# Kernel optimization log

Hardware: AMD Instinct MI355X
Metric: run time of the kernel (lower is better)

## Reference

```python
import jax, jax.numpy as jnp
import numpy as np
from jax.ops import segment_sum

N_NODES = 50000
N_EDGES = 150000
IN_FEATS = 512
OUT_FEATS = 512


def setup_inputs() -> dict:
    key = jax.random.key(0)
    k1, k2, k3, k4 = jax.random.split(key, 4)
    x = jax.random.normal(k1, (N_NODES, IN_FEATS), dtype=jnp.float32)
    src = jax.random.randint(k2, (N_EDGES,), 0, N_NODES, dtype=jnp.int64)
    dst = jax.random.randint(k3, (N_EDGES,), 0, N_NODES, dtype=jnp.int64)
    # Xavier-uniform init like reset_parameters
    limit = float(np.sqrt(6.0 / (IN_FEATS + OUT_FEATS)))
    W = jax.random.uniform(k4, (IN_FEATS, OUT_FEATS), dtype=jnp.float32,
                           minval=-limit, maxval=limit)
    b = jnp.zeros((OUT_FEATS,), dtype=jnp.float32)
    return {"x": x, "src": src, "dst": dst, "W": W, "b": b}


def reference(x, src, dst, W, b):
    # DGL GraphConv with norm='both':
    #   out = relu( D_dst^{-1/2} A D_src^{-1/2} X W + b )
    # Dropout is identity in eval mode (training=False).
    ones = jnp.ones((src.shape[0],), dtype=x.dtype)
    deg_out = segment_sum(ones, src, num_segments=N_NODES)  # source out-degree
    deg_in = segment_sum(ones, dst, num_segments=N_NODES)   # dest in-degree
    norm_src = jnp.where(deg_out > 0, deg_out, 1.0) ** -0.5  # [N]
    norm_dst = jnp.where(deg_in > 0, deg_in, 1.0) ** -0.5    # [N]

    h = x * norm_src[:, None]                         # [N, in]
    agg = segment_sum(h[src], dst, num_segments=N_NODES)  # scatter-add over edges
    agg = agg * norm_dst[:, None]                     # [N, in]
    out = agg @ W + b                                 # [N, out]
    return jax.nn.relu(out)
```

## Files before the change

kernel.cpp:

```cpp
#include <hip/hip_runtime.h>
#include <hip/hip_bf16.h>

#define N_NODES 50000
#define N_PAD   50048
#define N_EDGES 150000
#define F 512
#define BM 128
#define BN 128
#define BK 64
#define NBLK 196

typedef __attribute__((ext_vector_type(4))) float f32x4;
typedef __attribute__((ext_vector_type(4))) unsigned int u32x4;
typedef __attribute__((ext_vector_type(2))) unsigned int u32x2;

__device__ __forceinline__ unsigned short f2bf(float f) {
    unsigned int u = __float_as_uint(f);
    return (unsigned short)((u + 0x7fffu + ((u >> 16) & 1u)) >> 16);
}
__device__ __forceinline__ unsigned int pack2(float a, float b) {
    return (unsigned int)f2bf(a) | ((unsigned int)f2bf(b) << 16);
}
__device__ __forceinline__ void gload16(const void* g, void* l) {
    __builtin_amdgcn_global_load_lds(
        (const __attribute__((address_space(1))) unsigned int*)g,
        (__attribute__((address_space(3))) unsigned int*)l, 16, 0, 0);
}

__global__ void __launch_bounds__(256) crd_deg(const int* __restrict__ src,
                                               const int* __restrict__ dst,
                                               int* __restrict__ hist) {
    int e = blockIdx.x * 256 + threadIdx.x;
    if (e < N_EDGES) {
        atomicAdd(&hist[src[e]], 1);
        atomicAdd(&hist[N_NODES + dst[e]], 1);
    }
}

__global__ void __launch_bounds__(256) crd_norm(const int* __restrict__ hist,
                                                float* __restrict__ norms) {
    int i = blockIdx.x * 256 + threadIdx.x;
    if (i < 2 * N_NODES) {
        int d = hist[i];
        norms[i] = rsqrtf((float)(d > 0 ? d : 1));
    }
}

__global__ void __launch_bounds__(256) crd_bsum(const int* __restrict__ hist_in,
                                                int* __restrict__ bsum) {
    __shared__ int s[256];
    int t = threadIdx.x;
    int i = blockIdx.x * 256 + t;
    s[t] = (i < N_NODES) ? hist_in[i] : 0;
    __syncthreads();
    #pragma unroll
    for (int o = 128; o > 0; o >>= 1) {
        if (t < o) s[t] += s[t + o];
        __syncthreads();
    }
    if (t == 0) bsum[blockIdx.x] = s[0];
}

__global__ void __launch_bounds__(256) crd_bscan(const int* __restrict__ bsum,
                                                 int* __restrict__ bsumoff) {
    __shared__ int s[256];
    int t = threadIdx.x;
    int v = (t < NBLK) ? bsum[t] : 0;
    s[t] = v;
    __syncthreads();
    #pragma unroll
    for (int d = 1; d < 256; d <<= 1) {
        int add = (t >= d) ? s[t - d] : 0;
        __syncthreads();
        s[t] += add;
        __syncthreads();
    }
    if (t < NBLK) bsumoff[t] = s[t] - v;
}

__global__ void __launch_bounds__(256) crd_escan(const int* __restrict__ hist_in,
                                                 const int* __restrict__ bsumoff,
                                                 int* __restrict__ off,
                                                 int* __restrict__ cursor) {
    __shared__ int s[256];
    int t = threadIdx.x;
    int i = blockIdx.x * 256 + t;
    int v = (i < N_NODES) ? hist_in[i] : 0;
    s[t] = v;
    __syncthreads();
    #pragma unroll
    for (int d = 1; d < 256; d <<= 1) {
        int add = (t >= d) ? s[t - d] : 0;
        __syncthreads();
        s[t] += add;
        __syncthreads();
    }
    int excl = s[t] - v + bsumoff[blockIdx.x];
    if (i < N_NODES) { off[i] = excl; cursor[i] = excl; }
    if (i == N_NODES - 1) off[N_NODES] = excl + v;
}

__global__ void __launch_bounds__(256) crd_place(const int* __restrict__ src,
                                                 const int* __restrict__ dst,
                                                 int* __restrict__ cursor,
                                                 int* __restrict__ sorted) {
    int e = blockIdx.x * 256 + threadIdx.x;
    if (e < N_EDGES) {
        int slot = atomicAdd(&cursor[dst[e]], 1);
        sorted[slot] = src[e];
    }
}

__global__ void __launch_bounds__(256) crd_wt(const float* __restrict__ W,
                                              unsigned short* __restrict__ Wt) {
    int idx = blockIdx.x * 256 + threadIdx.x;
    int n = idx >> 9, k = idx & 511;
    Wt[idx] = f2bf(W[k * F + n]);
}

__global__ void __launch_bounds__(256) crd_xb(const float* __restrict__ x,
                                              unsigned short* __restrict__ xb) {
    size_t i = (size_t)(blockIdx.x * 256 + threadIdx.x) * 8;
    f32x4 v0 = *(const f32x4*)(x + i);
    f32x4 v1 = *(const f32x4*)(x + i + 4);
    u32x4 w;
    w.x = pack2(v0.x, v0.y); w.y = pack2(v0.z, v0.w);
    w.z = pack2(v1.x, v1.y); w.w = pack2(v1.z, v1.w);
    *(u32x4*)(xb + i) = w;
}

__global__ void __launch_bounds__(256) crd_gather_bf(const unsigned short* __restrict__ xb,
                                                     const int* __restrict__ sorted,
                                                     const int* __restrict__ off,
                                                     const float* __restrict__ norms,
                                                     unsigned short* __restrict__ aggb) {
    int wid = (blockIdx.x * 256 + threadIdx.x) >> 6;
    int lane = threadIdx.x & 63;
    if (wid >= N_PAD) return;
    float a0=0.f,a1=0.f,a2=0.f,a3=0.f,a4=0.f,a5=0.f,a6=0.f,a7=0.f;
    if (wid < N_NODES) {
        int e0 = off[wid], e1 = off[wid + 1];
        for (int e = e0; e < e1; ++e) {
            int s = sorted[e];
            float ns = norms[s];
            u32x4 v = *(const u32x4*)(xb + (size_t)s * F + lane * 8);
            a0 += __uint_as_float(v.x << 16) * ns;
            a1 += __uint_as_float(v.x & 0xffff0000u) * ns;
            a2 += __uint_as_float(v.y << 16) * ns;
            a3 += __uint_as_float(v.y & 0xffff0000u) * ns;
            a4 += __uint_as_float(v.z << 16) * ns;
            a5 += __uint_as_float(v.z & 0xffff0000u) * ns;
            a6 += __uint_as_float(v.w << 16) * ns;
            a7 += __uint_as_float(v.w & 0xffff0000u) * ns;
        }
        float nd = norms[N_NODES + wid];
        a0*=nd;a1*=nd;a2*=nd;a3*=nd;a4*=nd;a5*=nd;a6*=nd;a7*=nd;
    }
    u32x4 w;
    w.x = pack2(a0, a1); w.y = pack2(a2, a3);
    w.z = pack2(a4, a5); w.w = pack2(a6, a7);
    *(u32x4*)(aggb + (size_t)wid * F + lane * 8) = w;
}

__global__ void __launch_bounds__(256) crd_gather_f32(const float* __restrict__ x,
                                                      const int* __restrict__ sorted,
                                                      const int* __restrict__ off,
                                                      const float* __restrict__ norms,
                                                      unsigned short* __restrict__ aggb) {
    int wid = (blockIdx.x * 256 + threadIdx.x) >> 6;
    int lane = threadIdx.x & 63;
    if (wid >= N_PAD) return;
    f32x4 a0 = {0.f,0.f,0.f,0.f}, a1 = a0;
    if (wid < N_NODES) {
        int e0 = off[wid], e1 = off[wid + 1];
        for (int e = e0; e < e1; ++e) {
            int s = sorted[e];
            float ns = norms[s];
            const f32x4* p = (const f32x4*)(x + (size_t)s * F);
            a0 += p[lane] * ns;
            a1 += p[64 + lane] * ns;
        }
        float nd = norms[N_NODES + wid];
        a0 *= nd; a1 *= nd;
    }
    unsigned short* row = aggb + (size_t)wid * F;
    u32x2 w0, w1;
    w0.x = pack2(a0.x, a0.y); w0.y = pack2(a0.z, a0.w);
    w1.x = pack2(a1.x, a1.y); w1.y = pack2(a1.z, a1.w);
    *(u32x2*)(row + lane * 4) = w0;
    *(u32x2*)(row + 256 + lane * 4) = w1;
}

__global__ void __launch_bounds__(256, 3) crd_gemm(const unsigned short* __restrict__ aggb,
                                                   const unsigned short* __restrict__ Wt,
                                                   const float* __restrict__ bias,
                                                   float* __restrict__ out) {
    __shared__ __align__(16) unsigned short lA[8 * BM * 8];
    __shared__ __align__(16) unsigned short lB[8 * BN * 8];
    const int tid = threadIdx.x;
    const int rowbase = blockIdx.x * BM;
    const int nbase = blockIdx.y * BN;
    const int lane = tid & 63;
    const int wave = tid >> 6;
    const int wm = wave >> 1, wn = wave & 1;
    const int g = lane >> 4, r = lane & 15;

    f32x4 zero4 = {0.f, 0.f, 0.f, 0.f};
    f32x4 acc[4][4];
    #pragma unroll
    for (int i = 0; i < 4; ++i)
        #pragma unroll
        for (int j = 0; j < 4; ++j) acc[i][j] = zero4;

    for (int ks = 0; ks < F / BK; ++ks) {
        #pragma unroll
        for (int j = 0; j < 4; ++j) {
            int gg = (wave * 4 + j) * 64 + lane;
            int k8 = gg >> 7, row = gg & 127;
            gload16(aggb + (size_t)(rowbase + row) * F + ks * BK + k8 * 8,
                    &lA[(size_t)(wave * 4 + j) * 64 * 8]);
        }
        #pragma unroll
        for (int j = 0; j < 4; ++j) {
            int gg = (wave * 4 + j) * 64 + lane;
            int k8 = gg >> 7, n = gg & 127;
            gload16(Wt + (size_t)(nbase + n) * F + ks * BK + k8 * 8,
                    &lB[(size_t)(wave * 4 + j) * 64 * 8]);
        }
        __syncthreads();
        #pragma unroll
        for (int kk = 0; kk < 2; ++kk) {
            int k8 = kk * 4 + g;
            u32x4 af[4], bfr[4];
            #pragma unroll
            for (int mi = 0; mi < 4; ++mi)
                af[mi] = *(const u32x4*)&lA[(k8 * BM + wm * 64 + mi * 16 + r) * 8];
            #pragma unroll
            for (int ni = 0; ni < 4; ++ni)
                bfr[ni] = *(const u32x4*)&lB[(k8 * BN + wn * 64 + ni * 16 + r) * 8];
            #pragma unroll
            for (int mi = 0; mi < 4; ++mi)
                #pragma unroll
                for (int ni = 0; ni < 4; ++ni)
                    asm("v_mfma_f32_16x16x32_bf16 %0, %1, %2, %0"
                        : "+v"(acc[mi][ni])
                        : "v"(af[mi]), "v"(bfr[ni]));
        }
        __syncthreads();
    }
    #pragma unroll
    for (int ni = 0; ni < 4; ++ni) {
        int col = nbase + wn * 64 + ni * 16 + r;
        float bv = bias[col];
        #pragma unroll
        for (int mi = 0; mi < 4; ++mi) {
            #pragma unroll
            for (int j = 0; j < 4; ++j) {
                int row = rowbase + wm * 64 + mi * 16 + g * 4 + j;
                if (row < N_NODES) {
                    float v = acc[mi][ni][j] + bv;
                    out[(size_t)row * F + col] = v > 0.0f ? v : 0.0f;
                }
            }
        }
    }
}

extern "C" void kernel_launch(void* const* d_in, const int* in_sizes, int n_in,
                              void* d_out, int out_size, void* d_ws, size_t ws_size,
                              hipStream_t stream) {
    const float* x = (const float*)d_in[0];
    const int* src = (const int*)d_in[1];
    const int* dst = (const int*)d_in[2];
    const float* W = (const float*)d_in[3];
    const float* bias = (const float*)d_in[4];
    float* out = (float*)d_out;

    unsigned short* aggb = (unsigned short*)d_ws;
    unsigned short* Wt = aggb + (size_t)N_PAD * F;
    float* norms = (float*)(Wt + (size_t)F * F);
    int* hist = (int*)(norms + 2 * N_NODES);
    int* off = hist + 2 * N_NODES;
    int* cursor = off + N_NODES + 1;
    int* sorted = cursor + N_NODES;
    int* bsum = sorted + N_EDGES;
    int* bsumoff = bsum + NBLK;
    char* endp = (char*)(bsumoff + NBLK);
    unsigned short* xb = (unsigned short*)(((uintptr_t)endp + 63) & ~(uintptr_t)63);
    size_t need_min = (size_t)(endp - (char*)d_ws);
    size_t need_bf = (size_t)((char*)(xb + (size_t)N_NODES * F) - (char*)d_ws);
    if (ws_size < need_min) {
        hipMemsetAsync(d_out, 0, (size_t)out_size * sizeof(float), stream);
        return;
    }
    const bool use_bf = (ws_size >= need_bf);

    hipMemsetAsync(hist, 0, 2 * N_NODES * sizeof(int), stream);
    crd_deg<<<(N_EDGES + 255) / 256, 256, 0, stream>>>(src, dst, hist);
    crd_norm<<<(2 * N_NODES + 255) / 256, 256, 0, stream>>>(hist, norms);
    crd_bsum<<<NBLK, 256, 0, stream>>>(hist + N_NODES, bsum);
    crd_bscan<<<1, 256, 0, stream>>>(bsum, bsumoff);
    crd_escan<<<NBLK, 256, 0, stream>>>(hist + N_NODES, bsumoff, off, cursor);
    crd_wt<<<(F * F) / 256, 256, 0, stream>>>(W, Wt);
    crd_place<<<(N_EDGES + 255) / 256, 256, 0, stream>>>(src, dst, cursor, sorted);
    if (use_bf) {
        crd_xb<<<(int)(((size_t)N_NODES * F / 8) / 256), 256, 0, stream>>>(x, xb);
        crd_gather_bf<<<N_PAD / 4, 256, 0, stream>>>(xb, sorted, off, norms, aggb);
    } else {
        crd_gather_f32<<<N_PAD / 4, 256, 0, stream>>>(x, sorted, off, norms, aggb);
    }
    dim3 grid(N_PAD / BM, F / BN);
    crd_gemm<<<grid, 256, 0, stream>>>(aggb, Wt, bias, out);
}
```

Before: 186.1 us.

## Drop bf16 x pre-conversion, unroll fp32 gather, swizzle GEMM grid, vectorize epilogue

Removes the separate kernel that converted all of x to bf16 and instead gathers fp32 rows directly, unrolling the edge loop by two with independent accumulators to increase memory-level parallelism. The GEMM switches to a 1D grid remapped so each XCD handles a contiguous range of tiles, aiming for better L2 locality. Its MFMA operands are swapped so each lane holds four consecutive output columns, which allows 16-byte vectorized bias loads and output stores. The trade-off is reading fp32 rows during the gather (twice the bytes per edge) in exchange for skipping a full pass over x.

Result: faster. 165.9 us (-10.9%).

```diff
diff --git a/kernel.cpp b/kernel.cpp
--- a/kernel.cpp
+++ b/kernel.cpp
@@ -9,6 +9,7 @@
 #define BN 128
 #define BK 64
 #define NBLK 196
+#define NWG  1564
 
 typedef __attribute__((ext_vector_type(4))) float f32x4;
 typedef __attribute__((ext_vector_type(4))) unsigned int u32x4;
@@ -118,70 +119,35 @@
     Wt[idx] = f2bf(W[k * F + n]);
 }
 
-__global__ void __launch_bounds__(256) crd_xb(const float* __restrict__ x,
-                                              unsigned short* __restrict__ xb) {
-    size_t i = (size_t)(blockIdx.x * 256 + threadIdx.x) * 8;
-    f32x4 v0 = *(const f32x4*)(x + i);
-    f32x4 v1 = *(const f32x4*)(x + i + 4);
-    u32x4 w;
-    w.x = pack2(v0.x, v0.y); w.y = pack2(v0.z, v0.w);
-    w.z = pack2(v1.x, v1.y); w.w = pack2(v1.z, v1.w);
-    *(u32x4*)(xb + i) = w;
-}
-
-__global__ void __launch_bounds__(256) crd_gather_bf(const unsigned short* __restrict__ xb,
-                                                     const int* __restrict__ sorted,
-                                                     const int* __restrict__ off,
-                                                     const float* __restrict__ norms,
-                                                     unsigned short* __restrict__ aggb) {
+__global__ void __launch_bounds__(256) crd_gather(const float* __restrict__ x,
+                                                  const int* __restrict__ sorted,
+                                                  const int* __restrict__ off,
+                                                  const float* __restrict__ norms,
+                                                  unsigned short* __restrict__ aggb) {
     int wid = (blockIdx.x * 256 + threadIdx.x) >> 6;
     int lane = threadIdx.x & 63;
     if (wid >= N_PAD) return;
-    float a0=0.f,a1=0.f,a2=0.f,a3=0.f,a4=0.f,a5=0.f,a6=0.f,a7=0.f;
+    f32x4 a0 = {0.f,0.f,0.f,0.f}, a1 = a0, b0 = a0, b1 = a0;
     if (wid < N_NODES) {
         int e0 = off[wid], e1 = off[wid + 1];
-        for (int e = e0; e < e1; ++e) {
-            int s = sorted[e];
-            float ns = norms[s];
-            u32x4 v = *(const u32x4*)(xb + (size_t)s * F + lane * 8);
-            a0 += __uint_as_float(v.x << 16) * ns;
-            a1 += __uint_as_float(v.x & 0xffff0000u) * ns;
-            a2 += __uint_as_float(v.y << 16) * ns;
-            a3 += __uint_as_float(v.y & 0xffff0000u) * ns;
-            a4 += __uint_as_float(v.z << 16) * ns;
-            a5 += __uint_as_float(v.z & 0xffff0000u) * ns;
-            a6 += __uint_as_float(v.w << 16) * ns;
-            a7 += __uint_as_float(v.w & 0xffff0000u) * ns;
-        }
-        float nd = norms[N_NODES + wid];
-        a0*=nd;a1*=nd;a2*=nd;a3*=nd;a4*=nd;a5*=nd;a6*=nd;a7*=nd;
-    }
-    u32x4 w;
-    w.x = pack2(a0, a1); w.y = pack2(a2, a3);
-    w.z = pack2(a4, a5); w.w = pack2(a6, a7);
-    *(u32x4*)(aggb + (size_t)wid * F + lane * 8) = w;
-}
-
-__global__ void __launch_bounds__(256) crd_gather_f32(const float* __restrict__ x,
-                                                      const int* __restrict__ sorted,
-                                                      const int* __restrict__ off,
-                                                      const float* __restrict__ norms,
-                                                      unsigned short* __restrict__ aggb) {
-    int wid = (blockIdx.x * 256 + threadIdx.x) >> 6;
-    int lane = threadIdx.x & 63;
-    if (wid >= N_PAD) return;
-    f32x4 a0 = {0.f,0.f,0.f,0.f}, a1 = a0;
-    if (wid < N_NODES) {
-        int e0 = off[wid], e1 = off[wid + 1];
-        for (int e = e0; e < e1; ++e) {
+        int e = e0;
+        for (; e + 1 < e1; e += 2) {
+            int s0 = sorted[e], s1 = sorted[e + 1];
+            float ns0 = norms[s0], ns1 = norms[s1];
+            const f32x4* p0 = (const f32x4*)(x + (size_t)s0 * F);
+            const f32x4* p1 = (const f32x4*)(x + (size_t)s1 * F);
+            a0 += p0[lane] * ns0;  a1 += p0[64 + lane] * ns0;
+            b0 += p1[lane] * ns1;  b1 += p1[64 + lane] * ns1;
+        }
+        if (e < e1) {
             int s = sorted[e];
             float ns = norms[s];
             const f32x4* p = (const f32x4*)(x + (size_t)s * F);
-            a0 += p[lane] * ns;
-            a1 += p[64 + lane] * ns;
+            a0 += p[lane] * ns;  a1 += p[64 + lane] * ns;
         }
         float nd = norms[N_NODES + wid];
-        a0 *= nd; a1 *= nd;
+        a0 = (a0 + b0) * nd;
+        a1 = (a1 + b1) * nd;
     }
     unsigned short* row = aggb + (size_t)wid * F;
     u32x2 w0, w1;
@@ -198,19 +164,21 @@
     __shared__ __align__(16) unsigned short lA[8 * BM * 8];
     __shared__ __align__(16) unsigned short lB[8 * BN * 8];
     const int tid = threadIdx.x;
-    const int rowbase = blockIdx.x * BM;
-    const int nbase = blockIdx.y * BN;
+    int bid = blockIdx.x;
+    int xcd = bid & 7, lid = bid >> 3;
+    int swz = (xcd < 4 ? xcd * 196 : 784 + (xcd - 4) * 195) + lid;
+    const int rowbase = (swz >> 2) * BM;
+    const int nbase = (swz & 3) * BN;
     const int lane = tid & 63;
     const int wave = tid >> 6;
     const int wm = wave >> 1, wn = wave & 1;
     const int g = lane >> 4, r = lane & 15;
 
-    f32x4 zero4 = {0.f, 0.f, 0.f, 0.f};
     f32x4 acc[4][4];
     #pragma unroll
     for (int i = 0; i < 4; ++i)
         #pragma unroll
-        for (int j = 0; j < 4; ++j) acc[i][j] = zero4;
+        for (int j = 0; j < 4; ++j) acc[i][j] = (f32x4){0.f, 0.f, 0.f, 0.f};
 
     for (int ks = 0; ks < F / BK; ++ks) {
         #pragma unroll
@@ -243,24 +211,24 @@
                 #pragma unroll
                 for (int ni = 0; ni < 4; ++ni)
                     asm("v_mfma_f32_16x16x32_bf16 %0, %1, %2, %0"
-                        : "+v"(acc[mi][ni])
-                        : "v"(af[mi]), "v"(bfr[ni]));
-        }
-        __syncthreads();
-    }
-    #pragma unroll
-    for (int ni = 0; ni < 4; ++ni) {
-        int col = nbase + wn * 64 + ni * 16 + r;
-        float bv = bias[col];
-        #pragma unroll
-        for (int mi = 0; mi < 4; ++mi) {
-            #pragma unroll
-            for (int j = 0; j < 4; ++j) {
-                int row = rowbase + wm * 64 + mi * 16 + g * 4 + j;
-                if (row < N_NODES) {
-                    float v = acc[mi][ni][j] + bv;
-                    out[(size_t)row * F + col] = v > 0.0f ? v : 0.0f;
-                }
+                        : "+v"(acc[mi][ni]) : "v"(bfr[ni]), "v"(af[mi]));
+        }
+        __syncthreads();
+    }
+    #pragma unroll
+    for (int mi = 0; mi < 4; ++mi) {
+        int row = rowbase + wm * 64 + mi * 16 + r;
+        if (row < N_NODES) {
+            #pragma unroll
+            for (int ni = 0; ni < 4; ++ni) {
+                int c0 = nbase + wn * 64 + ni * 16 + g * 4;
+                f32x4 bv = *(const f32x4*)(bias + c0);
+                f32x4 v = acc[mi][ni] + bv;
+                v.x = v.x > 0.f ? v.x : 0.f;
+                v.y = v.y > 0.f ? v.y : 0.f;
+                v.z = v.z > 0.f ? v.z : 0.f;
+                v.w = v.w > 0.f ? v.w : 0.f;
+                *(f32x4*)(out + (size_t)row * F + c0) = v;
             }
         }
     }
@@ -285,15 +253,11 @@
     int* sorted = cursor + N_NODES;
     int* bsum = sorted + N_EDGES;
     int* bsumoff = bsum + NBLK;
-    char* endp = (char*)(bsumoff + NBLK);
-    unsigned short* xb = (unsigned short*)(((uintptr_t)endp + 63) & ~(uintptr_t)63);
-    size_t need_min = (size_t)(endp - (char*)d_ws);
-    size_t need_bf = (size_t)((char*)(xb + (size_t)N_NODES * F) - (char*)d_ws);
-    if (ws_size < need_min) {
+    size_t need = (size_t)((char*)(bsumoff + NBLK) - (char*)d_ws);
+    if (ws_size < need) {
         hipMemsetAsync(d_out, 0, (size_t)out_size * sizeof(float), stream);
         return;
     }
-    const bool use_bf = (ws_size >= need_bf);
 
     hipMemsetAsync(hist, 0, 2 * N_NODES * sizeof(int), stream);
     crd_deg<<<(N_EDGES + 255) / 256, 256, 0, stream>>>(src, dst, hist);
@@ -303,12 +267,6 @@
     crd_escan<<<NBLK, 256, 0, stream>>>(hist + N_NODES, bsumoff, off, cursor);
     crd_wt<<<(F * F) / 256, 256, 0, stream>>>(W, Wt);
     crd_place<<<(N_EDGES + 255) / 256, 256, 0, stream>>>(src, dst, cursor, sorted);
-    if (use_bf) {
-        crd_xb<<<(int)(((size_t)N_NODES * F / 8) / 256), 256, 0, stream>>>(x, xb);
-        crd_gather_bf<<<N_PAD / 4, 256, 0, stream>>>(xb, sorted, off, norms, aggb);
-    } else {
-        crd_gather_f32<<<N_PAD / 4, 256, 0, stream>>>(x, sorted, off, norms, aggb);
-    }
-    dim3 grid(N_PAD / BM, F / BN);
-    crd_gemm<<<grid, 256, 0, stream>>>(aggb, Wt, bias, out);
-}
+    crd_gather<<<N_PAD / 4, 256, 0, stream>>>(x, sorted, off, norms, aggb);
+    crd_gemm<<<NWG, 256, 0, stream>>>(aggb, Wt, bias, out);
+}
```
